# Performance work log

Measured on AMD Instinct MI355X. Metric: run time of the kernel, lower is better.

Reference implementation:

```python
import jax, jax.numpy as jnp
import numpy as np

NUM_CLASSES = 80
STRIDES = (8, 16, 32)
REG_WEIGHT = 5.0


def _decode(o, stride):
    # o: [B, 5+num_classes, H, W] -> [B, H*W, 5+num_classes] with grid decode
    B, C, H, W = o.shape
    o = o.reshape(B, C, H * W).transpose(0, 2, 1)  # [B, HW, C]
    yv, xv = jnp.meshgrid(jnp.arange(H), jnp.arange(W), indexing='ij')
    grid = jnp.stack([xv, yv], axis=-1).reshape(1, H * W, 2).astype(o.dtype)
    xy = (o[..., :2] + grid) * stride
    wh = jnp.exp(o[..., 2:4]) * stride
    return jnp.concatenate([xy, wh, o[..., 4:]], axis=-1)


def _iou_loss(pred, target):
    # pred, target: [N,4] in cxcywh; IOUloss(loss_type='iou'): 1 - iou**2
    tl = jnp.maximum(pred[:, :2] - pred[:, 2:] / 2, target[:, :2] - target[:, 2:] / 2)
    br = jnp.minimum(pred[:, :2] + pred[:, 2:] / 2, target[:, :2] + target[:, 2:] / 2)
    area_p = jnp.prod(pred[:, 2:], axis=1)
    area_g = jnp.prod(target[:, 2:], axis=1)
    en = jnp.prod((tl < br).astype(pred.dtype), axis=1)
    area_i = jnp.prod(br - tl, axis=1) * en
    area_u = area_p + area_g - area_i
    iou = area_i / (area_u + 1e-16)
    return 1.0 - iou ** 2


def _bce_logits(x, t):
    # numerically stable BCEWithLogitsLoss(reduction='none')
    return jnp.maximum(x, 0.0) - x * t + jnp.log1p(jnp.exp(-jnp.abs(x)))


def _total_loss(out0, out1, out2, reg_targets, cls_targets, fg):
    outs = jnp.concatenate(
        [_decode(o, s) for o, s in zip((out0, out1, out2), STRIDES)], axis=1)
    bbox_preds = outs[..., :4]      # [B, A, 4] decoded cxcywh
    obj_preds = outs[..., 4]        # [B, A] logits
    cls_preds = outs[..., 5:]       # [B, A, num_classes] logits
    B, A, _ = bbox_preds.shape
    num_fg = jnp.maximum(fg.sum(), 1.0)
    iou_l = _iou_loss(bbox_preds.reshape(-1, 4), reg_targets.reshape(-1, 4)).reshape(B, A)
    loss_iou = (iou_l * fg).sum() / num_fg
    loss_obj = _bce_logits(obj_preds, fg).sum() / num_fg
    loss_cls = (_bce_logits(cls_preds, cls_targets) * fg[..., None]).sum() / num_fg
    return REG_WEIGHT * loss_iou + loss_obj + loss_cls


def setup_inputs() -> dict:
    key = jax.random.key(0)
    ks = jax.random.split(key, 6)
    B = 32
    A = 80 * 80 + 40 * 40 + 20 * 20  # 8400 anchors for 640x640 input
    out0 = jax.random.normal(ks[0], (B, 85, 80, 80), dtype=jnp.float32)
    out1 = jax.random.normal(ks[1], (B, 85, 40, 40), dtype=jnp.float32)
    out2 = jax.random.normal(ks[2], (B, 85, 20, 20), dtype=jnp.float32)
    # cxcywh targets in image coords (640x640), wh strictly positive
    reg_targets = jax.random.uniform(ks[3], (B, A, 4), dtype=jnp.float32) * 300.0 + 1.0
    cls_targets = jax.random.uniform(ks[4], (B, A, 80), dtype=jnp.float32)
    fg_mask = jax.random.randint(ks[5], (B, A), 0, 2, dtype=jnp.int32)
    return {'out0': out0, 'out1': out1, 'out2': out2,
            'reg_targets': reg_targets, 'cls_targets': cls_targets,
            'fg_mask': fg_mask}


def reference(out0, out1, out2, reg_targets, cls_targets, fg_mask):
    fg = fg_mask.astype(out0.dtype)
    return _total_loss(out0, out1, out2, reg_targets, cls_targets, fg)
```

## Files before the change

### kernel.cpp

```cpp
#include <hip/hip_runtime.h>
#include <math.h>

constexpr int A_TOTAL = 8400;
constexpr int AGPI    = A_TOTAL / 4;

typedef float v4f __attribute__((ext_vector_type(4)));
typedef int   v4i __attribute__((ext_vector_type(4)));

__device__ __forceinline__ float bce(float x, float t) {
    float ax = fabsf(x);
    float sp = __logf(1.0f + __expf(-ax));
    return fmaxf(x, 0.0f) - x * t + sp;
}

__device__ __forceinline__ v4f ntload4(const float* p) {
    return __builtin_nontemporal_load(reinterpret_cast<const v4f*>(p));
}
__device__ __forceinline__ v4i ntloadi4(const int* p) {
    return __builtin_nontemporal_load(reinterpret_cast<const v4i*>(p));
}

__global__ __launch_bounds__(256) void yolox_fused(
    const float* __restrict__ out0, const float* __restrict__ out1,
    const float* __restrict__ out2, const float* __restrict__ regt,
    const float* __restrict__ clst, const int* __restrict__ fgm,
    double* __restrict__ acc, int B)
{
    int t  = blockIdx.x * blockDim.x + threadIdx.x;
    int q  = t & 3;
    int ag = t >> 2;
    int b  = ag / AGPI;
    int rg = ag - b * AGPI;
    int a0 = rg * 4;

    const float* obase; int HW; float stride; int al; int W;
    if (a0 < 6400)      { obase = out0 + (size_t)b * 85 * 6400; HW = 6400; stride = 8.0f;  al = a0;        W = 80; }
    else if (a0 < 8000) { obase = out1 + (size_t)b * 85 * 1600; HW = 1600; stride = 16.0f; al = a0 - 6400; W = 40; }
    else                { obase = out2 + (size_t)b * 85 * 400;  HW = 400;  stride = 32.0f; al = a0 - 8000; W = 20; }

    v4f L[20];
    const float* cb = obase + (size_t)(5 + q * 20) * HW + al;
    #pragma unroll
    for (int i = 0; i < 20; ++i)
        L[i] = ntload4(cb + (size_t)i * HW);

    v4i fg4 = ntloadi4(fgm + (size_t)b * A_TOTAL + a0);
    float fgf[4] = { (float)fg4.x, (float)fg4.y, (float)fg4.z, (float)fg4.w };

    float local = 0.0f;
    #pragma unroll
    for (int j = 0; j < 4; ++j) {
        const float* tp = clst + ((size_t)b * A_TOTAL + a0 + j) * 80 + q * 20;
        float tg[20];
        #pragma unroll
        for (int i5 = 0; i5 < 5; ++i5) {
            v4f tv = ntload4(tp + 4 * i5);
            tg[4 * i5 + 0] = tv.x; tg[4 * i5 + 1] = tv.y;
            tg[4 * i5 + 2] = tv.z; tg[4 * i5 + 3] = tv.w;
        }
        float s = 0.0f;
        #pragma unroll
        for (int i = 0; i < 20; ++i)
            s += bce(L[i][j], tg[i]);
        local += s * fgf[j];
    }

    {
        int aa  = al + q;
        int a   = a0 + q;
        int gx  = aa % W;
        int gy  = aa / W;
        float tx   = obase[aa];
        float ty   = obase[(size_t)1 * HW + aa];
        float tw   = obase[(size_t)2 * HW + aa];
        float th   = obase[(size_t)3 * HW + aa];
        float tobj = obase[(size_t)4 * HW + aa];

        float px = (tx + (float)gx) * stride;
        float py = (ty + (float)gy) * stride;
        float pw = __expf(tw) * stride;
        float ph = __expf(th) * stride;

        v4f rt = ntload4(regt + ((size_t)b * A_TOTAL + a) * 4);
        float fgv = fgf[q];

        float tlx = fmaxf(px - pw * 0.5f, rt.x - rt.z * 0.5f);
        float tly = fmaxf(py - ph * 0.5f, rt.y - rt.w * 0.5f);
        float brx = fminf(px + pw * 0.5f, rt.x + rt.z * 0.5f);
        float bry = fminf(py + ph * 0.5f, rt.y + rt.w * 0.5f);
        float area_p = pw * ph;
        float area_g = rt.z * rt.w;
        float en = ((tlx < brx) && (tly < bry)) ? 1.0f : 0.0f;
        float area_i = (brx - tlx) * (bry - tly) * en;
        float area_u = area_p + area_g - area_i;
        float iou = area_i / (area_u + 1e-16f);
        float l_iou = 1.0f - iou * iou;

        local += 5.0f * l_iou * fgv + bce(tobj, fgv);
        float fgl = fgv;

        for (int off = 32; off > 0; off >>= 1) {
            local += __shfl_down(local, off, 64);
            fgl   += __shfl_down(fgl,   off, 64);
        }
        __shared__ float s_v[4], s_w[4];
        int wid  = threadIdx.x >> 6;
        int lane = threadIdx.x & 63;
        if (lane == 0) { s_v[wid] = local; s_w[wid] = fgl; }
        __syncthreads();
        if (threadIdx.x == 0) {
            atomicAdd(&acc[0], (double)(s_v[0] + s_v[1] + s_v[2] + s_v[3]));
            atomicAdd(&acc[1], (double)(s_w[0] + s_w[1] + s_w[2] + s_w[3]));
        }
    }
}

__global__ void yolox_final(const double* __restrict__ acc, float* __restrict__ out) {
    out[0] = (float)(acc[0] / fmax(acc[1], 1.0));
}

extern "C" void kernel_launch(void* const* d_in, const int* in_sizes, int n_in,
                              void* d_out, int out_size, void* d_ws, size_t ws_size,
                              hipStream_t stream) {
    const float* out0 = (const float*)d_in[0];
    const float* out1 = (const float*)d_in[1];
    const float* out2 = (const float*)d_in[2];
    const float* regt = (const float*)d_in[3];
    const float* clst = (const float*)d_in[4];
    const int*   fgm  = (const int*)d_in[5];

    int B = in_sizes[0] / (85 * 6400);
    double* acc = (double*)d_ws;
    (void)hipMemsetAsync(acc, 0, 2 * sizeof(double), stream);

    int total  = B * A_TOTAL;
    int blocks = (total + 255) / 256;
    hipLaunchKernelGGL(yolox_fused, dim3(blocks), dim3(256), 0, stream,
                       out0, out1, out2, regt, clst, fgm, acc, B);
    hipLaunchKernelGGL(yolox_final, dim3(1), dim3(1), 0, stream, acc, (float*)d_out);
}
```

Before: 225.2 us.

## Double-buffer class logit and target loads in chunks with plain loads

Replaces the up-front load of all 20 logit vectors plus per-anchor target loads with a five-step, double-buffered chunk loop. Each step prefetches the next 4 logit rows and 4 target vectors while computing BCE on the current ones. Box and objectness loads are hoisted to the start, nontemporal loads become ordinary loads, and launch bounds request 4 blocks per CU. The goal is lower register pressure, higher occupancy and better latency hiding, at the cost of less memory-level parallelism per thread and a different cache policy.

```diff
diff --git a/kernel.cpp b/kernel.cpp
--- a/kernel.cpp
+++ b/kernel.cpp
@@ -13,14 +13,22 @@
     return fmaxf(x, 0.0f) - x * t + sp;
 }
 
-__device__ __forceinline__ v4f ntload4(const float* p) {
-    return __builtin_nontemporal_load(reinterpret_cast<const v4f*>(p));
-}
-__device__ __forceinline__ v4i ntloadi4(const int* p) {
-    return __builtin_nontemporal_load(reinterpret_cast<const v4i*>(p));
+__device__ __forceinline__ v4f ld4(const float* p) {
+    return *reinterpret_cast<const v4f*>(p);
 }
 
-__global__ __launch_bounds__(256) void yolox_fused(
+__device__ __forceinline__ void consume_chunk(const v4f (&L)[4], const v4f (&T)[4],
+                                              float& a0, float& a1, float& a2, float& a3) {
+    #pragma unroll
+    for (int c = 0; c < 4; ++c) {
+        a0 += bce(L[c][0], T[0][c]);
+        a1 += bce(L[c][1], T[1][c]);
+        a2 += bce(L[c][2], T[2][c]);
+        a3 += bce(L[c][3], T[3][c]);
+    }
+}
+
+__global__ __launch_bounds__(256, 4) void yolox_fused(
     const float* __restrict__ out0, const float* __restrict__ out1,
     const float* __restrict__ out2, const float* __restrict__ regt,
     const float* __restrict__ clst, const int* __restrict__ fgm,
@@ -31,87 +39,91 @@
     int ag = t >> 2;
     int b  = ag / AGPI;
     int rg = ag - b * AGPI;
-    int a0 = rg * 4;
+    int a0i = rg * 4;
 
     const float* obase; int HW; float stride; int al; int W;
-    if (a0 < 6400)      { obase = out0 + (size_t)b * 85 * 6400; HW = 6400; stride = 8.0f;  al = a0;        W = 80; }
-    else if (a0 < 8000) { obase = out1 + (size_t)b * 85 * 1600; HW = 1600; stride = 16.0f; al = a0 - 6400; W = 40; }
-    else                { obase = out2 + (size_t)b * 85 * 400;  HW = 400;  stride = 32.0f; al = a0 - 8000; W = 20; }
+    if (a0i < 6400)      { obase = out0 + (size_t)b * 85 * 6400; HW = 6400; stride = 8.0f;  al = a0i;        W = 80; }
+    else if (a0i < 8000) { obase = out1 + (size_t)b * 85 * 1600; HW = 1600; stride = 16.0f; al = a0i - 6400; W = 40; }
+    else                 { obase = out2 + (size_t)b * 85 * 400;  HW = 400;  stride = 32.0f; al = a0i - 8000; W = 20; }
 
-    v4f L[20];
-    const float* cb = obase + (size_t)(5 + q * 20) * HW + al;
+    const float* cb    = obase + (size_t)(5 + q * 20) * HW + al;
+    const float* tbase = clst + ((size_t)b * A_TOTAL + a0i) * 80 + q * 20;
+
+    int aa = al + q;
+    float tx   = obase[aa];
+    float ty   = obase[(size_t)1 * HW + aa];
+    float tw   = obase[(size_t)2 * HW + aa];
+    float th   = obase[(size_t)3 * HW + aa];
+    float tobj = obase[(size_t)4 * HW + aa];
+    v4f rt  = ld4(regt + ((size_t)b * A_TOTAL + a0i + q) * 4);
+    v4i fg4 = *reinterpret_cast<const v4i*>(fgm + (size_t)b * A_TOTAL + a0i);
+
+    v4f L0[4], L1[4], T0[4], T1[4];
     #pragma unroll
-    for (int i = 0; i < 20; ++i)
-        L[i] = ntload4(cb + (size_t)i * HW);
+    for (int i = 0; i < 4; ++i) L0[i] = ld4(cb + (size_t)i * HW);
+    #pragma unroll
+    for (int j = 0; j < 4; ++j) T0[j] = ld4(tbase + (size_t)j * 80);
 
-    v4i fg4 = ntloadi4(fgm + (size_t)b * A_TOTAL + a0);
-    float fgf[4] = { (float)fg4.x, (float)fg4.y, (float)fg4.z, (float)fg4.w };
+    float s0 = 0.f, s1 = 0.f, s2 = 0.f, s3 = 0.f;
 
-    float local = 0.0f;
     #pragma unroll
-    for (int j = 0; j < 4; ++j) {
-        const float* tp = clst + ((size_t)b * A_TOTAL + a0 + j) * 80 + q * 20;
-        float tg[20];
-        #pragma unroll
-        for (int i5 = 0; i5 < 5; ++i5) {
-            v4f tv = ntload4(tp + 4 * i5);
-            tg[4 * i5 + 0] = tv.x; tg[4 * i5 + 1] = tv.y;
-            tg[4 * i5 + 2] = tv.z; tg[4 * i5 + 3] = tv.w;
+    for (int k = 0; k < 5; ++k) {
+        if (k < 4) {
+            if ((k & 1) == 0) {
+                #pragma unroll
+                for (int i = 0; i < 4; ++i) L1[i] = ld4(cb + (size_t)(4 * (k + 1) + i) * HW);
+                #pragma unroll
+                for (int j = 0; j < 4; ++j) T1[j] = ld4(tbase + (size_t)j * 80 + 4 * (k + 1));
+            } else {
+                #pragma unroll
+                for (int i = 0; i < 4; ++i) L0[i] = ld4(cb + (size_t)(4 * (k + 1) + i) * HW);
+                #pragma unroll
+                for (int j = 0; j < 4; ++j) T0[j] = ld4(tbase + (size_t)j * 80 + 4 * (k + 1));
+            }
         }
-        float s = 0.0f;
-        #pragma unroll
-        for (int i = 0; i < 20; ++i)
-            s += bce(L[i][j], tg[i]);
-        local += s * fgf[j];
+        if ((k & 1) == 0) consume_chunk(L0, T0, s0, s1, s2, s3);
+        else              consume_chunk(L1, T1, s0, s1, s2, s3);
     }
 
-    {
-        int aa  = al + q;
-        int a   = a0 + q;
-        int gx  = aa % W;
-        int gy  = aa / W;
-        float tx   = obase[aa];
-        float ty   = obase[(size_t)1 * HW + aa];
-        float tw   = obase[(size_t)2 * HW + aa];
-        float th   = obase[(size_t)3 * HW + aa];
-        float tobj = obase[(size_t)4 * HW + aa];
+    float fgf0 = (float)fg4.x, fgf1 = (float)fg4.y, fgf2 = (float)fg4.z, fgf3 = (float)fg4.w;
+    float local = s0 * fgf0 + s1 * fgf1 + s2 * fgf2 + s3 * fgf3;
 
-        float px = (tx + (float)gx) * stride;
-        float py = (ty + (float)gy) * stride;
-        float pw = __expf(tw) * stride;
-        float ph = __expf(th) * stride;
+    int gx = aa % W;
+    int gy = aa / W;
+    float px = (tx + (float)gx) * stride;
+    float py = (ty + (float)gy) * stride;
+    float pw = __expf(tw) * stride;
+    float ph = __expf(th) * stride;
 
-        v4f rt = ntload4(regt + ((size_t)b * A_TOTAL + a) * 4);
-        float fgv = fgf[q];
+    float fgv = q == 0 ? fgf0 : (q == 1 ? fgf1 : (q == 2 ? fgf2 : fgf3));
 
-        float tlx = fmaxf(px - pw * 0.5f, rt.x - rt.z * 0.5f);
-        float tly = fmaxf(py - ph * 0.5f, rt.y - rt.w * 0.5f);
-        float brx = fminf(px + pw * 0.5f, rt.x + rt.z * 0.5f);
-        float bry = fminf(py + ph * 0.5f, rt.y + rt.w * 0.5f);
-        float area_p = pw * ph;
-        float area_g = rt.z * rt.w;
-        float en = ((tlx < brx) && (tly < bry)) ? 1.0f : 0.0f;
-        float area_i = (brx - tlx) * (bry - tly) * en;
-        float area_u = area_p + area_g - area_i;
-        float iou = area_i / (area_u + 1e-16f);
-        float l_iou = 1.0f - iou * iou;
+    float tlx = fmaxf(px - pw * 0.5f, rt.x - rt.z * 0.5f);
+    float tly = fmaxf(py - ph * 0.5f, rt.y - rt.w * 0.5f);
+    float brx = fminf(px + pw * 0.5f, rt.x + rt.z * 0.5f);
+    float bry = fminf(py + ph * 0.5f, rt.y + rt.w * 0.5f);
+    float area_p = pw * ph;
+    float area_g = rt.z * rt.w;
+    float en = ((tlx < brx) && (tly < bry)) ? 1.0f : 0.0f;
+    float area_i = (brx - tlx) * (bry - tly) * en;
+    float area_u = area_p + area_g - area_i;
+    float iou = area_i / (area_u + 1e-16f);
+    float l_iou = 1.0f - iou * iou;
 
-        local += 5.0f * l_iou * fgv + bce(tobj, fgv);
-        float fgl = fgv;
+    local += 5.0f * l_iou * fgv + bce(tobj, fgv);
+    float fgl = fgv;
 
-        for (int off = 32; off > 0; off >>= 1) {
-            local += __shfl_down(local, off, 64);
-            fgl   += __shfl_down(fgl,   off, 64);
-        }
-        __shared__ float s_v[4], s_w[4];
-        int wid  = threadIdx.x >> 6;
-        int lane = threadIdx.x & 63;
-        if (lane == 0) { s_v[wid] = local; s_w[wid] = fgl; }
-        __syncthreads();
-        if (threadIdx.x == 0) {
-            atomicAdd(&acc[0], (double)(s_v[0] + s_v[1] + s_v[2] + s_v[3]));
-            atomicAdd(&acc[1], (double)(s_w[0] + s_w[1] + s_w[2] + s_w[3]));
-        }
+    for (int off = 32; off > 0; off >>= 1) {
+        local += __shfl_down(local, off, 64);
+        fgl   += __shfl_down(fgl,   off, 64);
+    }
+    __shared__ float s_v[4], s_w[4];
+    int wid  = threadIdx.x >> 6;
+    int lane = threadIdx.x & 63;
+    if (lane == 0) { s_v[wid] = local; s_w[wid] = fgl; }
+    __syncthreads();
+    if (threadIdx.x == 0) {
+        atomicAdd(&acc[0], (double)(s_v[0] + s_v[1] + s_v[2] + s_v[3]));
+        atomicAdd(&acc[1], (double)(s_w[0] + s_w[1] + s_w[2] + s_w[3]));
     }
 }
 
```

New measurement: 257.6 us. 1.14x slower.
